# Kernel optimization log

Hardware: AMD Instinct MI355X
Metric: run time of the kernel (lower is better)

Reference implementation:

```python
import jax, jax.numpy as jnp
import numpy as np

H = 2048
E = 8
K = 2
INTER = 2048
T = 2048


def setup_inputs() -> dict:
    key = jax.random.key(0)
    k1, k2, k3 = jax.random.split(key, 3)
    hidden_4d = jax.random.normal(k1, (1, 1, T, H), dtype=jnp.float32)
    # learned per-expert fused gate+up projection: [1, E, H, 2*inter]
    gate_up_proj = jax.random.normal(k2, (1, E, H, INTER * 2), dtype=jnp.float32) * 0.02
    # binary (expert, token) dispatch mask: on average K of E experts active per token
    sparsity = (jax.random.uniform(k3, (1, E, T, 1)) < (K / E)).astype(jnp.float32)
    return {"hidden_4d": hidden_4d, "gate_up_proj": gate_up_proj, "sparsity": sparsity}


def reference(hidden_4d, gate_up_proj, sparsity):
    # sparse_matmul semantics: per-expert GEMM of tokens against expert weight
    # blocks, with output blocks zeroed (skipped) where the sparsity mask is 0.
    # hidden_4d: [1, 1, T, H]; gate_up_proj: [1, E, H, F]; sparsity: [1, E, T, 1]
    # out[a, e, t, f] = mask[a, e, t] * sum_h hidden[a, 0, t, h] * W[a, e, h, f]
    out = jnp.einsum("abth,aehf->aetf", hidden_4d, gate_up_proj) * sparsity
    return out.sum()
```

## Files before the change

### kernel.cpp

```cpp
#include <hip/hip_runtime.h>

#define H_DIM 2048
#define E_DIM 8
#define T_DIM 2048
#define F_DIM 4096
#define ROWS (E_DIM * H_DIM)
#define TCHUNK 512
#define TCHUNKS 4
#define A_BLOCKS 8
#define RS_BLOCKS (ROWS / 4)

typedef float f32x4 __attribute__((ext_vector_type(4)));


__global__ __launch_bounds__(256) void fused_compute(
    const float* __restrict__ hidden,
    const float* __restrict__ W,
    const float* __restrict__ mask,
    float* __restrict__ ws,
    float* __restrict__ out) {
  float* Bsum = ws;
  float* Ap   = ws + ROWS;
  int bid = blockIdx.x;
  int tid = threadIdx.x;

  if (bid < A_BLOCKS) {
    if (bid == 0 && tid == 0) out[0] = 0.f;

    int hb = bid & 1;
    int tc = bid >> 1;
    int t0 = tc * TCHUNK;
    int h4 = hb * 1024 + tid * 4;

    __shared__ float m_lds[E_DIM][TCHUNK];
    #pragma unroll
    for (int i = 0; i < (E_DIM * TCHUNK) / 256; ++i) {
      int idx = i * 256 + tid;
      int e = idx >> 9, tt = idx & 511;
      m_lds[e][tt] = mask[e * T_DIM + t0 + tt];
    }
    __syncthreads();

    f32x4 acc[E_DIM];
    #pragma unroll
    for (int e = 0; e < E_DIM; ++e) acc[e] = (f32x4)0.f;
    #pragma unroll 2
    for (int t = 0; t < TCHUNK; ++t) {
      f32x4 hv = *(const f32x4*)(hidden + (size_t)(t0 + t) * H_DIM + h4);
      #pragma unroll
      for (int e = 0; e < E_DIM; ++e)
        acc[e] += hv * m_lds[e][t];
    }
    #pragma unroll
    for (int e = 0; e < E_DIM; ++e)
      *(f32x4*)(Ap + (size_t)tc * ROWS + e * H_DIM + h4) = acc[e];
  } else {
    int row  = ((bid - A_BLOCKS) << 2) | (tid >> 6);
    int lane = tid & 63;
    const f32x4* rp = (const f32x4*)(W + (size_t)row * F_DIM);
    float s = 0.f;
    #pragma unroll
    for (int i = 0; i < 16; ++i) {
      f32x4 v = __builtin_nontemporal_load(rp + lane + (i << 6));
      s += (v.x + v.y) + (v.z + v.w);
    }
    #pragma unroll
    for (int off = 32; off > 0; off >>= 1)
      s += __shfl_down(s, off, 64);
    if (lane == 0) Bsum[row] = s;
  }
}

__global__ __launch_bounds__(1024) void dot_kernel(const float* __restrict__ ws,
                                                   float* __restrict__ out) {
  const f32x4* B4 = (const f32x4*)ws;
  const f32x4* A4 = (const f32x4*)(ws + ROWS);
  int i = blockIdx.x * 1024 + threadIdx.x;

  f32x4 a = (A4[i] + A4[4096 + i]) + (A4[8192 + i] + A4[12288 + i]);
  f32x4 b = B4[i];
  float s = (a.x * b.x + a.y * b.y) + (a.z * b.z + a.w * b.w);

  #pragma unroll
  for (int off = 32; off > 0; off >>= 1)
    s += __shfl_down(s, off, 64);

  __shared__ float red[16];
  int wave = threadIdx.x >> 6;
  int lane = threadIdx.x & 63;
  if (lane == 0) red[wave] = s;
  __syncthreads();
  if (threadIdx.x == 0) {
    float r = 0.f;
    #pragma unroll
    for (int w = 0; w < 16; ++w) r += red[w];
    atomicAdd(out, r);
  }
}

extern "C" void kernel_launch(void* const* d_in, const int* in_sizes, int n_in,
                              void* d_out, int out_size, void* d_ws, size_t ws_size,
                              hipStream_t stream) {
  const float* hidden = (const float*)d_in[0];
  const float* W      = (const float*)d_in[1];
  const float* mask   = (const float*)d_in[2];
  float* out = (float*)d_out;
  float* ws  = (float*)d_ws;

  fused_compute<<<A_BLOCKS + RS_BLOCKS, 256, 0, stream>>>(hidden, W, mask, ws, out);
  dot_kernel<<<4, 1024, 0, stream>>>(ws, out);
}
```

Measured before the change: 469.4 us.

## Split mask-weighted token sum into more chunks and batch row sums per wave

```diff
diff --git a/kernel.cpp b/kernel.cpp
--- a/kernel.cpp
+++ b/kernel.cpp
@@ -5,10 +5,12 @@
 #define T_DIM 2048
 #define F_DIM 4096
 #define ROWS (E_DIM * H_DIM)
-#define TCHUNK 512
-#define TCHUNKS 4
-#define A_BLOCKS 8
-#define RS_BLOCKS (ROWS / 4)
+#define TCHUNK 128
+#define TCHUNKS 16
+#define A_BLOCKS 32
+#define RS_BLOCKS 1024
+#define RS_WAVES (RS_BLOCKS * 4)
+#define ROWS_PER_WAVE (ROWS / RS_WAVES)
 
 typedef float f32x4 __attribute__((ext_vector_type(4)));
 
@@ -36,7 +38,7 @@
     #pragma unroll
     for (int i = 0; i < (E_DIM * TCHUNK) / 256; ++i) {
       int idx = i * 256 + tid;
-      int e = idx >> 9, tt = idx & 511;
+      int e = idx >> 7, tt = idx & 127;
       m_lds[e][tt] = mask[e * T_DIM + t0 + tt];
     }
     __syncthreads();
@@ -55,19 +57,30 @@
     for (int e = 0; e < E_DIM; ++e)
       *(f32x4*)(Ap + (size_t)tc * ROWS + e * H_DIM + h4) = acc[e];
   } else {
-    int row  = ((bid - A_BLOCKS) << 2) | (tid >> 6);
+    int wv   = ((bid - A_BLOCKS) << 2) | (tid >> 6);
     int lane = tid & 63;
-    const f32x4* rp = (const f32x4*)(W + (size_t)row * F_DIM);
-    float s = 0.f;
+    float s[ROWS_PER_WAVE];
     #pragma unroll
-    for (int i = 0; i < 16; ++i) {
-      f32x4 v = __builtin_nontemporal_load(rp + lane + (i << 6));
-      s += (v.x + v.y) + (v.z + v.w);
+    for (int rr = 0; rr < ROWS_PER_WAVE; ++rr) {
+      int row = wv + rr * RS_WAVES;
+      const f32x4* rp = (const f32x4*)(W + (size_t)row * F_DIM);
+      f32x4 a = (f32x4)0.f;
+      #pragma unroll
+      for (int i = 0; i < 16; ++i)
+        a += rp[lane + (i << 6)];
+      s[rr] = (a.x + a.y) + (a.z + a.w);
     }
     #pragma unroll
-    for (int off = 32; off > 0; off >>= 1)
-      s += __shfl_down(s, off, 64);
-    if (lane == 0) Bsum[row] = s;
+    for (int off = 32; off > 0; off >>= 1) {
+      #pragma unroll
+      for (int rr = 0; rr < ROWS_PER_WAVE; ++rr)
+        s[rr] += __shfl_down(s[rr], off, 64);
+    }
+    if (lane == 0) {
+      #pragma unroll
+      for (int rr = 0; rr < ROWS_PER_WAVE; ++rr)
+        Bsum[wv + rr * RS_WAVES] = s[rr];
+    }
   }
 }
 
@@ -77,7 +90,10 @@
   const f32x4* A4 = (const f32x4*)(ws + ROWS);
   int i = blockIdx.x * 1024 + threadIdx.x;
 
-  f32x4 a = (A4[i] + A4[4096 + i]) + (A4[8192 + i] + A4[12288 + i]);
+  f32x4 a = (f32x4)0.f;
+  #pragma unroll
+  for (int c = 0; c < TCHUNKS; ++c)
+    a += A4[(size_t)c * (ROWS / 4) + i];
   f32x4 b = B4[i];
   float s = (a.x * b.x + a.y * b.y) + (a.z * b.z + a.w * b.w);
 
```

After: 388.6 us. 1.21x faster.
